# Kernel optimization log

Hardware: AMD Instinct MI355X
Metric: run time of the kernel (lower is better)

The kernel has to match this reference:

```python
import jax, jax.numpy as jnp
import numpy as np

H, D_MODEL, DK, DV = 16, 1024, 64, 64
B, S = 4, 2048
LN_EPS = 1e-6
NEG = -1e9


def setup_inputs() -> dict:
    key = jax.random.key(0)
    ks = jax.random.split(key, 8)
    query = jax.random.normal(ks[0], (B, S, D_MODEL), dtype=jnp.float32)
    k_in = jax.random.normal(ks[1], (B, S, D_MODEL), dtype=jnp.float32)
    v_in = jax.random.normal(ks[2], (B, S, D_MODEL), dtype=jnp.float32)
    mask = jax.random.randint(ks[3], (B, S, S), 0, 2, dtype=jnp.int32)
    sc = 1.0 / np.sqrt(D_MODEL)
    w_qs = jax.random.normal(ks[4], (D_MODEL, H * DK), dtype=jnp.float32) * sc
    w_ks = jax.random.normal(ks[5], (D_MODEL, H * DK), dtype=jnp.float32) * sc
    w_vs = jax.random.normal(ks[6], (D_MODEL, H * DV), dtype=jnp.float32) * sc
    w_out = jax.random.normal(ks[7], (H * DV, D_MODEL), dtype=jnp.float32) * (1.0 / np.sqrt(H * DV))
    ln_g = jnp.ones((D_MODEL,), dtype=jnp.float32)
    ln_b = jnp.zeros((D_MODEL,), dtype=jnp.float32)
    return {"query": query, "key": k_in, "value": v_in, "mask": mask,
            "w_qs": w_qs, "w_ks": w_ks, "w_vs": w_vs, "w_out": w_out,
            "ln_g": ln_g, "ln_b": ln_b}


def reference(query, key, value, mask, w_qs, w_ks, w_vs, w_out, ln_g, ln_b):
    # projections -> [B, H, S, dk/dv]
    q = (query @ w_qs).reshape(B, S, H, DK).transpose(0, 2, 1, 3)
    k = (key @ w_ks).reshape(B, S, H, DK).transpose(0, 2, 1, 3)
    v = (value @ w_vs).reshape(B, S, H, DV).transpose(0, 2, 1, 3)
    scores = jnp.einsum('bhqd,bhkd->bhqk', q, k) / np.sqrt(DK)
    scores = jnp.where(mask[:, None, :, :] == 0, NEG, scores)
    p = jax.nn.softmax(scores, axis=-1)  # dropout = identity in eval
    x = jnp.einsum('bhqk,bhkd->bhqd', p, v)  # [B,H,S,DV]
    x = x.transpose(0, 2, 1, 3).reshape(B, S, H * DV)
    out = x @ w_out + query  # dropout identity, residual
    mu = out.mean(-1, keepdims=True)
    var = out.var(-1, keepdims=True)
    return (out - mu) / jnp.sqrt(var + LN_EPS) * ln_g + ln_b
```

## Files before the change

### kernel.cpp

```cpp
#include <hip/hip_runtime.h>

#define BB   4
#define SS   2048
#define HH   16
#define DM   1024
#define DKV  64
#define LNEPS 1e-6f

#define MD_BF16 0
#define MD_F32  1
#define MD_F16  2

typedef __attribute__((ext_vector_type(8))) short bf16x8;
typedef __attribute__((ext_vector_type(4))) float f32x4;
#define MFMA16(a,b,c) __builtin_amdgcn_mfma_f32_16x16x32_bf16(a,b,c,0,0,0)

__device__ __forceinline__ void gl_lds16(const ushort* g, ushort* l) {
    __builtin_amdgcn_global_load_lds(
        (const __attribute__((address_space(1))) void*)g,
        (__attribute__((address_space(3))) void*)l, 16, 0, 0);
}
__device__ __forceinline__ void wait_vm0_barrier() {
    asm volatile("s_waitcnt vmcnt(0)" ::: "memory");
    __builtin_amdgcn_s_barrier();
}

__device__ __forceinline__ float2 unpack2(unsigned int u) {
    union { unsigned int i; float f; } a, b;
    a.i = u << 16;
    b.i = u & 0xffff0000u;
    return make_float2(a.f, b.f);
}
__device__ __forceinline__ unsigned short f2bf(float f) {
    union { float f; unsigned int i; } c; c.f = f;
    unsigned int u = c.i;
    unsigned int r = u + 0x7fffu + ((u >> 16) & 1u);
    return (unsigned short)(r >> 16);
}
__device__ __forceinline__ unsigned short f2bf_t(float f) {
    union { float f; unsigned int i; } c; c.f = f;
    return (unsigned short)(c.i >> 16);
}
__device__ __forceinline__ float h2f(unsigned int bits16) {
    unsigned short s = (unsigned short)bits16;
    _Float16 x;
    __builtin_memcpy(&x, &s, 2);
    return (float)x;
}
__device__ __forceinline__ void load8m(const void* p, int mode, size_t e0, float* o) {
    if (mode == MD_F32) {
        const float* f = (const float*)p + e0;
        float4 a = *(const float4*)f;
        float4 b = *(const float4*)(f + 4);
        o[0] = a.x; o[1] = a.y; o[2] = a.z; o[3] = a.w;
        o[4] = b.x; o[5] = b.y; o[6] = b.z; o[7] = b.w;
    } else {
        uint4 u = *(const uint4*)((const ushort*)p + e0);
        unsigned v[4] = {u.x, u.y, u.z, u.w};
        if (mode == MD_BF16) {
#pragma unroll
            for (int j = 0; j < 4; ++j) { float2 t = unpack2(v[j]); o[2*j] = t.x; o[2*j+1] = t.y; }
        } else {
#pragma unroll
            for (int j = 0; j < 4; ++j) { o[2*j] = h2f(v[j] & 0xFFFFu); o[2*j+1] = h2f(v[j] >> 16); }
        }
    }
}
__device__ __forceinline__ void load4m(const void* p, int mode, size_t e0, float* o) {
    if (mode == MD_F32) {
        float4 v = *(const float4*)((const float*)p + e0);
        o[0] = v.x; o[1] = v.y; o[2] = v.z; o[3] = v.w;
    } else {
        uint2 u = *(const uint2*)((const ushort*)p + e0);
        if (mode == MD_BF16) {
            float2 a = unpack2(u.x), b = unpack2(u.y);
            o[0] = a.x; o[1] = a.y; o[2] = b.x; o[3] = b.y;
        } else {
            o[0] = h2f(u.x & 0xFFFFu); o[1] = h2f(u.x >> 16);
            o[2] = h2f(u.y & 0xFFFFu); o[3] = h2f(u.y >> 16);
        }
    }
}
__device__ __forceinline__ float loadS(const void* p, int mode, size_t i) {
    if (mode == MD_F32) return ((const float*)p)[i];
    unsigned short u = ((const ushort*)p)[i];
    if (mode == MD_BF16) { union { unsigned i; float f; } c; c.i = (unsigned)u << 16; return c.f; }
    return h2f(u);
}

struct SniffArgs { const void* p[10]; int nhalf[10]; };

__global__ void sniff_all(SniffArgs a, int* __restrict__ modes) {
    __shared__ int cE, cO;
    const int slots[9] = {0, 1, 2, 4, 5, 6, 7, 8, 9};
    const int slot = slots[blockIdx.x];
    const ushort* p = (const ushort*)a.p[slot];
    const int nhalf = a.nhalf[slot];
    if (threadIdx.x == 0) { cE = 0; cO = 0; }
    __syncthreads();
    int e = 0, o = 0;
    for (int i = threadIdx.x; i < nhalf; i += 256) {
        unsigned ex = (p[i] >> 7) & 0xFFu;
        int hit = (ex < 100u || ex == 0xFFu) ? 1 : 0;
        if (i & 1) o += hit; else e += hit;
    }
    atomicAdd(&cE, e);
    atomicAdd(&cO, o);
    __syncthreads();
    if (threadIdx.x == 0) {
        int total = cE + cO;
        modes[slot] = (total < 48) ? MD_BF16 : ((cO * 4 < cE) ? MD_F32 : MD_F16);
    }
}

__global__ __launch_bounds__(256) void mpack(
    const int* __restrict__ mask, unsigned int* __restrict__ pm)
{
    const int w = blockIdx.x * 256 + threadIdx.x;
    const int* p = mask + (size_t)w * 32;
    unsigned int bits = 0u;
#pragma unroll
    for (int j = 0; j < 8; ++j) {
        int4 v = *(const int4*)(p + j * 4);
        bits |= (v.x ? 1u : 0u) << (4 * j);
        bits |= (v.y ? 1u : 0u) << (4 * j + 1);
        bits |= (v.z ? 1u : 0u) << (4 * j + 2);
        bits |= (v.w ? 1u : 0u) << (4 * j + 3);
    }
    pm[w] = bits;
}

__global__ __launch_bounds__(256) void aconv(
    const void* __restrict__ A, ushort* __restrict__ Ab,
    const int* __restrict__ modes, int slot)
{
    const int m = modes[slot];
    const size_t e0 = ((size_t)blockIdx.x * 256 + threadIdx.x) * 16;
    float t[16];
    load8m(A, m, e0, t);
    load8m(A, m, e0 + 8, t + 8);
    union { ushort u[16]; uint4 v[2]; } p;
#pragma unroll
    for (int j = 0; j < 16; ++j) p.u[j] = f2bf(t[j]);
    *(uint4*)&Ab[e0]     = p.v[0];
    *(uint4*)&Ab[e0 + 8] = p.v[1];
}

struct WtArgs { const void* W[3]; ushort* Wt[3]; int slot[3]; };

__device__ __forceinline__ void wtrans_body(
    const void* __restrict__ W, ushort* __restrict__ Wt, int m)
{
    __shared__ ushort T[64][68];
    const int tid = threadIdx.x;
    const int k0 = blockIdx.y * 64, n0 = blockIdx.x * 64;

    const int r = tid >> 2, c = (tid & 3) * 16;
    float t[4];
#pragma unroll
    for (int j = 0; j < 4; ++j) {
        load4m(W, m, (size_t)(k0 + r) * DM + n0 + c + 4 * j, t);
#pragma unroll
        for (int i = 0; i < 4; ++i) T[r][c + 4 * j + i] = f2bf(t[i]);
    }
    __syncthreads();

    const int rn = tid >> 2, ck = (tid & 3) * 16;
    union { ushort u[8]; uint4 v; } p0, p1;
#pragma unroll
    for (int j = 0; j < 8; ++j) { p0.u[j] = T[ck + j][rn]; p1.u[j] = T[ck + 8 + j][rn]; }
    ushort* op = &Wt[(size_t)(n0 + rn) * DM + k0 + ck];
    *(uint4*)op = p0.v;
    *(uint4*)(op + 8) = p1.v;
}

__global__ __launch_bounds__(256) void wtrans3(WtArgs a, const int* __restrict__ modes) {
    const int g = blockIdx.z;
    wtrans_body(a.W[g], a.Wt[g], modes[a.slot[g]]);
}
__global__ __launch_bounds__(256) void wtrans(
    const void* __restrict__ W, ushort* __restrict__ Wt,
    const int* __restrict__ modes, int wslot)
{
    wtrans_body(W, Wt, modes[wslot]);
}

__global__ __launch_bounds__(256) void proj_mfma(
    const ushort* __restrict__ A, const ushort* __restrict__ Wt,
    ushort* __restrict__ Out, int vmode, float scale)
{
    __shared__ __align__(16) ushort Asf[2][4096];
    __shared__ __align__(16) ushort Bsf[2][4096];

    const int tid = threadIdx.x;
    const int lane = tid & 63, wv = tid >> 6;
    const int quad = lane >> 4, L = lane & 15;
    const int bid = blockIdx.y * gridDim.x + blockIdx.x;
    const int swz = (bid & 7) * 64 + (bid >> 3);
    const int m0 = (swz >> 3) * 128, n0 = (swz & 7) * 128;
    const int wm = (wv >> 1) * 64, wn = (wv & 1) * 64;

    const int e0 = (wv * 2 + 0) * 512 + lane * 8;
    const int e1 = (wv * 2 + 1) * 512 + lane * 8;
    const ushort* gA0 = A  + (size_t)(m0 + (e0 >> 5)) * DM + (e0 & 31);
    const ushort* gA1 = A  + (size_t)(m0 + (e1 >> 5)) * DM + (e1 & 31);
    const ushort* gB0 = Wt + (size_t)(n0 + (e0 >> 5)) * DM + (e0 & 31);
    const ushort* gB1 = Wt + (size_t)(n0 + (e1 >> 5)) * DM + (e1 & 31);

    f32x4 acc[4][4];
#pragma unroll
    for (int i = 0; i < 4; ++i)
#pragma unroll
        for (int j = 0; j < 4; ++j) { acc[i][j][0] = 0.f; acc[i][j][1] = 0.f; acc[i][j][2] = 0.f; acc[i][j][3] = 0.f; }

    gl_lds16(gA0, &Asf[0][e0]);
    gl_lds16(gA1, &Asf[0][e1]);
    gl_lds16(gB0, &Bsf[0][e0]);
    gl_lds16(gB1, &Bsf[0][e1]);
    wait_vm0_barrier();

    int cur = 0;
    for (int kt = 0; kt < 31; ++kt) {
        const int kn = (kt + 1) * 32;
        gl_lds16(gA0 + kn, &Asf[cur ^ 1][e0]);
        gl_lds16(gA1 + kn, &Asf[cur ^ 1][e1]);
        gl_lds16(gB0 + kn, &Bsf[cur ^ 1][e0]);
        gl_lds16(gB1 + kn, &Bsf[cur ^ 1][e1]);

        bf16x8 af[4], bfr[4];
#pragma unroll
        for (int tm = 0; tm < 4; ++tm) af[tm] = *(const bf16x8*)&Asf[cur][(wm + tm * 16 + L) * 32 + quad * 8];
#pragma unroll
        for (int tn = 0; tn < 4; ++tn) bfr[tn] = *(const bf16x8*)&Bsf[cur][(wn + tn * 16 + L) * 32 + quad * 8];
#pragma unroll
        for (int tm = 0; tm < 4; ++tm)
#pragma unroll
            for (int tn = 0; tn < 4; ++tn)
                acc[tm][tn] = MFMA16(af[tm], bfr[tn], acc[tm][tn]);

        wait_vm0_barrier();
        cur ^= 1;
    }
    {
        bf16x8 af[4], bfr[4];
#pragma unroll
        for (int tm = 0; tm < 4; ++tm) af[tm] = *(const bf16x8*)&Asf[cur][(wm + tm * 16 + L) * 32 + quad * 8];
#pragma unroll
        for (int tn = 0; tn < 4; ++tn) bfr[tn] = *(const bf16x8*)&Bsf[cur][(wn + tn * 16 + L) * 32 + quad * 8];
#pragma unroll
        for (int tm = 0; tm < 4; ++tm)
#pragma unroll
            for (int tn = 0; tn < 4; ++tn)
                acc[tm][tn] = MFMA16(af[tm], bfr[tn], acc[tm][tn]);
    }

#pragma unroll
    for (int tm = 0; tm < 4; ++tm)
#pragma unroll
        for (int tn = 0; tn < 4; ++tn)
#pragma unroll
            for (int r = 0; r < 4; ++r) {
                const int mm = m0 + wm + tm * 16 + quad * 4 + r;
                const int n = n0 + wn + tn * 16 + L;
                const int b = mm >> 11, s = mm & 2047;
                const int h = n >> 6, d = n & 63;
                const size_t o = vmode
                    ? ((size_t)(b * HH + h) * DKV + d) * SS + s
                    : ((size_t)(b * HH + h) * SS + s) * DKV + d;
                Out[o] = f2bf(acc[tm][tn][r] * scale);
            }
}

__global__ __launch_bounds__(256) void attn_mfma(
    const ushort* __restrict__ Q, const ushort* __restrict__ K,
    const ushort* __restrict__ Vt, const unsigned int* __restrict__ pm,
    ushort* __restrict__ Xo)
{
    __shared__ __align__(16) ushort Ks[64][72];
    __shared__ __align__(16) ushort Vs[64][72];
    __shared__ __align__(16) ushort Ps[64][72];

    const int tid = threadIdx.x;
    const int lane = tid & 63, wv = tid >> 6;
    const int quad = lane >> 4, L = lane & 15;
    const int bid = blockIdx.y * gridDim.x + blockIdx.x;
    const int swz = (bid & 7) * 256 + (bid >> 3);
    const int bh = swz >> 5, b = bh >> 4, h = bh & 15;
    const int q0 = (swz & 31) * 64;

    const ushort* qp = &Q[((size_t)bh * SS + q0 + wv * 16 + L) * DKV + quad * 8];
    const bf16x8 aq0 = *(const bf16x8*)qp;
    const bf16x8 aq1 = *(const bf16x8*)(qp + 32);

    f32x4 O[4];
    float lacc[4];
#pragma unroll
    for (int t = 0; t < 4; ++t) { O[t][0] = 0.f; O[t][1] = 0.f; O[t][2] = 0.f; O[t][3] = 0.f; }
#pragma unroll
    for (int r = 0; r < 4; ++r) lacc[r] = 0.f;

    const int sr = tid >> 2, sg = tid & 3;
    const ushort* kbase = &K[((size_t)bh * SS + sr) * DKV + sg * 16];
    const ushort* vbase = &Vt[((size_t)bh * DKV + sr) * SS + sg * 16];
    const unsigned int* pmr[4];
#pragma unroll
    for (int r = 0; r < 4; ++r)
        pmr[r] = pm + ((size_t)b * SS + q0 + wv * 16 + quad * 4 + r) * 64;

    for (int kt = 0; kt < 32; ++kt) {
        __syncthreads();
        *(uint4*)&Ks[sr][sg * 16]     = *(const uint4*)kbase;
        *(uint4*)&Ks[sr][sg * 16 + 8] = *(const uint4*)(kbase + 8);
        *(uint4*)&Vs[sr][sg * 16]     = *(const uint4*)vbase;
        *(uint4*)&Vs[sr][sg * 16 + 8] = *(const uint4*)(vbase + 8);
        kbase += 64 * DKV;
        vbase += 64;

        uint2 mw[4];
#pragma unroll
        for (int r = 0; r < 4; ++r) mw[r] = *(const uint2*)(pmr[r] + 2 * kt);

        __syncthreads();

        f32x4 sc[4];
        __builtin_amdgcn_s_setprio(1);
#pragma unroll
        for (int t = 0; t < 4; ++t) {
            bf16x8 b0 = *(const bf16x8*)&Ks[t * 16 + L][quad * 8];
            bf16x8 b1 = *(const bf16x8*)&Ks[t * 16 + L][32 + quad * 8];
            f32x4 c; c[0] = 0.f; c[1] = 0.f; c[2] = 0.f; c[3] = 0.f;
            c = MFMA16(aq0, b0, c);
            c = MFMA16(aq1, b1, c);
            sc[t] = c;
        }
        __builtin_amdgcn_s_setprio(0);

#pragma unroll
        for (int r = 0; r < 4; ++r) {
            const unsigned mx = mw[r].x, my = mw[r].y;
#pragma unroll
            for (int t = 0; t < 4; ++t) {
                const float s = fminf(sc[t][r], 30.f);
                const float e = __expf(s);
                const unsigned wsel = (t & 2) ? my : mx;
                const float p = ((wsel >> ((t & 1) * 16 + L)) & 1u) ? e : 0.f;
                lacc[r] += p;
                Ps[wv * 16 + quad * 4 + r][t * 16 + L] = f2bf_t(p);
            }
        }

        bf16x8 ap0 = *(const bf16x8*)&Ps[wv * 16 + L][quad * 8];
        bf16x8 ap1 = *(const bf16x8*)&Ps[wv * 16 + L][32 + quad * 8];
        __builtin_amdgcn_s_setprio(1);
#pragma unroll
        for (int t = 0; t < 4; ++t) {
            bf16x8 v0 = *(const bf16x8*)&Vs[t * 16 + L][quad * 8];
            bf16x8 v1 = *(const bf16x8*)&Vs[t * 16 + L][32 + quad * 8];
            O[t] = MFMA16(ap0, v0, O[t]);
            O[t] = MFMA16(ap1, v1, O[t]);
        }
        __builtin_amdgcn_s_setprio(0);
    }

    float inv[4];
#pragma unroll
    for (int r = 0; r < 4; ++r) {
        float l = lacc[r];
#pragma unroll
        for (int off = 1; off < 16; off <<= 1) l += __shfl_xor(l, off, 64);
        inv[r] = 1.f / l;
    }
#pragma unroll
    for (int t = 0; t < 4; ++t)
#pragma unroll
        for (int r = 0; r < 4; ++r) {
            const int qg = q0 + wv * 16 + quad * 4 + r;
            Xo[((size_t)b * SS + qg) * DM + h * DKV + t * 16 + L] = f2bf(O[t][r] * inv[r]);
        }
}

__global__ __launch_bounds__(256) void oproj_mfma(
    const ushort* __restrict__ Xin, const ushort* __restrict__ Wt,
    const void* __restrict__ Qres, float* __restrict__ Out,
    const int* __restrict__ modes)
{
    __shared__ __align__(16) ushort Asf[2][4096];
    __shared__ __align__(16) ushort Bsf[2][4096];

    const int tid = threadIdx.x;
    const int lane = tid & 63, wv = tid >> 6;
    const int quad = lane >> 4, L = lane & 15;
    const int bid = blockIdx.y * gridDim.x + blockIdx.x;
    const int swz = (bid & 7) * 64 + (bid >> 3);
    const int m0 = (swz >> 3) * 128, n0 = (swz & 7) * 128;
    const int wm = (wv >> 1) * 64, wn = (wv & 1) * 64;
    const int mq = modes[0];

    const int e0 = (wv * 2 + 0) * 512 + lane * 8;
    const int e1 = (wv * 2 + 1) * 512 + lane * 8;
    const ushort* gA0 = Xin + (size_t)(m0 + (e0 >> 5)) * DM + (e0 & 31);
    const ushort* gA1 = Xin + (size_t)(m0 + (e1 >> 5)) * DM + (e1 & 31);
    const ushort* gB0 = Wt  + (size_t)(n0 + (e0 >> 5)) * DM + (e0 & 31);
    const ushort* gB1 = Wt  + (size_t)(n0 + (e1 >> 5)) * DM + (e1 & 31);

    f32x4 acc[4][4];
#pragma unroll
    for (int i = 0; i < 4; ++i)
#pragma unroll
        for (int j = 0; j < 4; ++j) { acc[i][j][0] = 0.f; acc[i][j][1] = 0.f; acc[i][j][2] = 0.f; acc[i][j][3] = 0.f; }

    gl_lds16(gA0, &Asf[0][e0]);
    gl_lds16(gA1, &Asf[0][e1]);
    gl_lds16(gB0, &Bsf[0][e0]);
    gl_lds16(gB1, &Bsf[0][e1]);
    wait_vm0_barrier();

    int cur = 0;
    for (int kt = 0; kt < 31; ++kt) {
        const int kn = (kt + 1) * 32;
        gl_lds16(gA0 + kn, &Asf[cur ^ 1][e0]);
        gl_lds16(gA1 + kn, &Asf[cur ^ 1][e1]);
        gl_lds16(gB0 + kn, &Bsf[cur ^ 1][e0]);
        gl_lds16(gB1 + kn, &Bsf[cur ^ 1][e1]);

        bf16x8 af[4], bfr[4];
#pragma unroll
        for (int tm = 0; tm < 4; ++tm) af[tm] = *(const bf16x8*)&Asf[cur][(wm + tm * 16 + L) * 32 + quad * 8];
#pragma unroll
        for (int tn = 0; tn < 4; ++tn) bfr[tn] = *(const bf16x8*)&Bsf[cur][(wn + tn * 16 + L) * 32 + quad * 8];
#pragma unroll
        for (int tm = 0; tm < 4; ++tm)
#pragma unroll
            for (int tn = 0; tn < 4; ++tn)
                acc[tm][tn] = MFMA16(af[tm], bfr[tn], acc[tm][tn]);

        wait_vm0_barrier();
        cur ^= 1;
    }
    {
        bf16x8 af[4], bfr[4];
#pragma unroll
        for (int tm = 0; tm < 4; ++tm) af[tm] = *(const bf16x8*)&Asf[cur][(wm + tm * 16 + L) * 32 + quad * 8];
#pragma unroll
        for (int tn = 0; tn < 4; ++tn) bfr[tn] = *(const bf16x8*)&Bsf[cur][(wn + tn * 16 + L) * 32 + quad * 8];
#pragma unroll
        for (int tm = 0; tm < 4; ++tm)
#pragma unroll
            for (int tn = 0; tn < 4; ++tn)
                acc[tm][tn] = MFMA16(af[tm], bfr[tn], acc[tm][tn]);
    }

#pragma unroll
    for (int tm = 0; tm < 4; ++tm)
#pragma unroll
        for (int tn = 0; tn < 4; ++tn)
#pragma unroll
            for (int r = 0; r < 4; ++r) {
                const int mm = m0 + wm + tm * 16 + quad * 4 + r;
                const int n = n0 + wn + tn * 16 + L;
                const size_t idx = (size_t)mm * DM + n;
                Out[idx] = acc[tm][tn][r] + loadS(Qres, mq, idx);
            }
}

__global__ __launch_bounds__(256) void ln_k(
    float* __restrict__ Out, const void* __restrict__ G,
    const void* __restrict__ Bt, const int* __restrict__ modes)
{
    const int tid = threadIdx.x, wv = tid >> 6, lane = tid & 63;
    const int row = blockIdx.x * 4 + wv;
    const int mg = modes[8], mb = modes[9];
    const size_t base = (size_t)row * DM + lane * 16;

    float v[16];
    float s = 0.f, q = 0.f;
#pragma unroll
    for (int j = 0; j < 16; j += 4) {
        float4 t = *(const float4*)&Out[base + j];
        v[j] = t.x; v[j+1] = t.y; v[j+2] = t.z; v[j+3] = t.w;
        s += t.x + t.y + t.z + t.w;
        q += t.x*t.x + t.y*t.y + t.z*t.z + t.w*t.w;
    }
#pragma unroll
    for (int off = 1; off < 64; off <<= 1) {
        s += __shfl_xor(s, off, 64);
        q += __shfl_xor(q, off, 64);
    }
    const float mu = s * (1.f / 1024.f);
    const float var = q * (1.f / 1024.f) - mu * mu;
    const float inv = rsqrtf(var + LNEPS);

    float gj[16], bj[16];
#pragma unroll
    for (int j = 0; j < 16; j += 4) {
        load4m(G,  mg, (size_t)lane * 16 + j, gj + j);
        load4m(Bt, mb, (size_t)lane * 16 + j, bj + j);
    }
#pragma unroll
    for (int j = 0; j < 16; j += 4) {
        float4 o;
        o.x = (v[j]   - mu) * inv * gj[j]   + bj[j];
        o.y = (v[j+1] - mu) * inv * gj[j+1] + bj[j+1];
        o.z = (v[j+2] - mu) * inv * gj[j+2] + bj[j+2];
        o.w = (v[j+3] - mu) * inv * gj[j+3] + bj[j+3];
        *(float4*)&Out[base + j] = o;
    }
}

extern "C" void kernel_launch(void* const* d_in, const int* in_sizes, int n_in,
                              void* d_out, int out_size, void* d_ws, size_t ws_size,
                              hipStream_t stream)
{
    const void* query = d_in[0];
    const void* key_i = d_in[1];
    const void* value = d_in[2];
    const int*  mask  = (const int*)d_in[3];
    const void* w_qs  = d_in[4];
    const void* w_ks  = d_in[5];
    const void* w_vs  = d_in[6];
    const void* w_out = d_in[7];
    const void* ln_g  = d_in[8];
    const void* ln_b  = d_in[9];
    float* out = (float*)d_out;

    int* modes = (int*)d_ws;
    const size_t PE = (size_t)BB * HH * SS * DKV;
    ushort* Qw = (ushort*)((char*)d_ws + 256);
    ushort* Kw = Qw + PE;
    ushort* Vw = Kw + PE;
    ushort* Xw = Vw + PE;
    ushort* Abuf = Xw;
    ushort* Wtq  = (ushort*)((char*)d_out + (4  << 20));
    ushort* Wtk  = (ushort*)((char*)d_out + (8  << 20));
    ushort* Wtv  = (ushort*)((char*)d_out + (12 << 20));
    ushort* Wt2  = Qw;
    unsigned int* pmask = (unsigned int*)d_out;

    SniffArgs sa;
    for (int i = 0; i < 10; ++i) {
        sa.p[i] = d_in[i];
        sa.nhalf[i] = in_sizes[i] < 4096 ? in_sizes[i] : 4096;
    }
    sniff_all<<<9, 256, 0, stream>>>(sa, modes);
    mpack<<<2048, 256, 0, stream>>>(mask, pmask);

    WtArgs wa;
    wa.W[0] = w_qs; wa.Wt[0] = Wtq; wa.slot[0] = 4;
    wa.W[1] = w_ks; wa.Wt[1] = Wtk; wa.slot[1] = 5;
    wa.W[2] = w_vs; wa.Wt[2] = Wtv; wa.slot[2] = 6;
    wtrans3<<<dim3(16, 16, 3), 256, 0, stream>>>(wa, modes);

    dim3 gproj(8, 64), gtr(16, 16);

    aconv<<<2048, 256, 0, stream>>>(query, Abuf, modes, 0);
    proj_mfma<<<gproj, 256, 0, stream>>>(Abuf, Wtq, Qw, 0, 0.125f);

    aconv<<<2048, 256, 0, stream>>>(key_i, Abuf, modes, 1);
    proj_mfma<<<gproj, 256, 0, stream>>>(Abuf, Wtk, Kw, 0, 1.0f);

    aconv<<<2048, 256, 0, stream>>>(value, Abuf, modes, 2);
    proj_mfma<<<gproj, 256, 0, stream>>>(Abuf, Wtv, Vw, 1, 1.0f);

    attn_mfma<<<dim3(32, 64), 256, 0, stream>>>(Qw, Kw, Vw, pmask, Xw);

    wtrans<<<gtr, 256, 0, stream>>>(w_out, Wt2, modes, 7);
    oproj_mfma<<<gproj, 256, 0, stream>>>(Xw, Wt2, query, out, modes);
    ln_k<<<2048, 256, 0, stream>>>(out, ln_g, ln_b, modes);
}
```

Measured before the change: 527.1 us.

## Fuse input bf16 conversion into QKV projection and batch three GEMMs in one launch

The separate aconv kernels, which converted each activation tensor to a bf16 buffer, are removed. The projection GEMM now loads raw fp32/bf16/fp16 activations into registers, converts them, and stores them to padded LDS, overlapping the next tile's load with the current MFMAs. The Q, K and V projections run as one launch using grid z, which drops two launches and the bf16 round-trip through global memory. In exchange, the A operand no longer goes through direct global-to-LDS loads, register pressure rises from the 16-float staging, and launch bounds now request 4 blocks per CU.

Result: slower. 541.9 us (+2.8%).

```diff
diff --git a/kernel.cpp b/kernel.cpp
--- a/kernel.cpp
+++ b/kernel.cpp
@@ -46,25 +46,6 @@
     _Float16 x;
     __builtin_memcpy(&x, &s, 2);
     return (float)x;
-}
-__device__ __forceinline__ void load8m(const void* p, int mode, size_t e0, float* o) {
-    if (mode == MD_F32) {
-        const float* f = (const float*)p + e0;
-        float4 a = *(const float4*)f;
-        float4 b = *(const float4*)(f + 4);
-        o[0] = a.x; o[1] = a.y; o[2] = a.z; o[3] = a.w;
-        o[4] = b.x; o[5] = b.y; o[6] = b.z; o[7] = b.w;
-    } else {
-        uint4 u = *(const uint4*)((const ushort*)p + e0);
-        unsigned v[4] = {u.x, u.y, u.z, u.w};
-        if (mode == MD_BF16) {
-#pragma unroll
-            for (int j = 0; j < 4; ++j) { float2 t = unpack2(v[j]); o[2*j] = t.x; o[2*j+1] = t.y; }
-        } else {
-#pragma unroll
-            for (int j = 0; j < 4; ++j) { o[2*j] = h2f(v[j] & 0xFFFFu); o[2*j+1] = h2f(v[j] >> 16); }
-        }
-    }
 }
 __device__ __forceinline__ void load4m(const void* p, int mode, size_t e0, float* o) {
     if (mode == MD_F32) {
@@ -88,6 +69,35 @@
     return h2f(u);
 }
 
+__device__ __forceinline__ void loadAraw(const void* p, int m, size_t e, uint4* r) {
+    if (m == MD_F32) {
+        const float* f = (const float*)p + e;
+        r[0] = *(const uint4*)(f);
+        r[1] = *(const uint4*)(f + 4);
+        r[2] = *(const uint4*)(f + 8);
+        r[3] = *(const uint4*)(f + 12);
+    } else {
+        const ushort* s = (const ushort*)p + e;
+        r[0] = *(const uint4*)s;
+        r[1] = *(const uint4*)(s + 8);
+    }
+}
+__device__ __forceinline__ void cvtA16(const uint4* r, int m, uint4* o2) {
+    union { ushort u[16]; uint4 v[2]; } o;
+    if (m == MD_F32) {
+        const float* f = (const float*)r;
+#pragma unroll
+        for (int j = 0; j < 16; ++j) o.u[j] = f2bf(f[j]);
+    } else if (m == MD_BF16) {
+        o.v[0] = r[0]; o.v[1] = r[1];
+    } else {
+        const ushort* s = (const ushort*)r;
+#pragma unroll
+        for (int j = 0; j < 16; ++j) o.u[j] = f2bf(h2f(s[j]));
+    }
+    o2[0] = o.v[0]; o2[1] = o.v[1];
+}
+
 struct SniffArgs { const void* p[10]; int nhalf[10]; };
 
 __global__ void sniff_all(SniffArgs a, int* __restrict__ modes) {
@@ -130,22 +140,6 @@
     pm[w] = bits;
 }
 
-__global__ __launch_bounds__(256) void aconv(
-    const void* __restrict__ A, ushort* __restrict__ Ab,
-    const int* __restrict__ modes, int slot)
-{
-    const int m = modes[slot];
-    const size_t e0 = ((size_t)blockIdx.x * 256 + threadIdx.x) * 16;
-    float t[16];
-    load8m(A, m, e0, t);
-    load8m(A, m, e0 + 8, t + 8);
-    union { ushort u[16]; uint4 v[2]; } p;
-#pragma unroll
-    for (int j = 0; j < 16; ++j) p.u[j] = f2bf(t[j]);
-    *(uint4*)&Ab[e0]     = p.v[0];
-    *(uint4*)&Ab[e0 + 8] = p.v[1];
-}
-
 struct WtArgs { const void* W[3]; ushort* Wt[3]; int slot[3]; };
 
 __device__ __forceinline__ void wtrans_body(
@@ -185,12 +179,22 @@
     wtrans_body(W, Wt, modes[wslot]);
 }
 
-__global__ __launch_bounds__(256) void proj_mfma(
-    const ushort* __restrict__ A, const ushort* __restrict__ Wt,
-    ushort* __restrict__ Out, int vmode, float scale)
-{
-    __shared__ __align__(16) ushort Asf[2][4096];
-    __shared__ __align__(16) ushort Bsf[2][4096];
+__global__ __launch_bounds__(256, 4) void projqkv(
+    const void* __restrict__ Aq, const void* __restrict__ Ak, const void* __restrict__ Av,
+    const ushort* __restrict__ Wtq, const ushort* __restrict__ Wtk, const ushort* __restrict__ Wtv,
+    ushort* __restrict__ Qo, ushort* __restrict__ Ko, ushort* __restrict__ Vo,
+    const int* __restrict__ modes)
+{
+    __shared__ __align__(16) ushort As[2][128 * 40];
+    __shared__ __align__(16) ushort Bs[2][128 * 32];
+
+    const int z = blockIdx.z;
+    const void* A = (z == 0) ? Aq : (z == 1) ? Ak : Av;
+    const ushort* Wt = (z == 0) ? Wtq : (z == 1) ? Wtk : Wtv;
+    ushort* Out = (z == 0) ? Qo : (z == 1) ? Ko : Vo;
+    const int vmode = (z == 2);
+    const float scale = (z == 0) ? 0.125f : 1.0f;
+    const int m = modes[z];
 
     const int tid = threadIdx.x;
     const int lane = tid & 63, wv = tid >> 6;
@@ -202,51 +206,63 @@
 
     const int e0 = (wv * 2 + 0) * 512 + lane * 8;
     const int e1 = (wv * 2 + 1) * 512 + lane * 8;
-    const ushort* gA0 = A  + (size_t)(m0 + (e0 >> 5)) * DM + (e0 & 31);
-    const ushort* gA1 = A  + (size_t)(m0 + (e1 >> 5)) * DM + (e1 & 31);
     const ushort* gB0 = Wt + (size_t)(n0 + (e0 >> 5)) * DM + (e0 & 31);
     const ushort* gB1 = Wt + (size_t)(n0 + (e1 >> 5)) * DM + (e1 & 31);
 
+    const int arow = tid >> 1, aseg = tid & 1;
+    const size_t aoff = (size_t)(m0 + arow) * DM + aseg * 16;
+    const int alds = arow * 40 + aseg * 16;
+
     f32x4 acc[4][4];
 #pragma unroll
     for (int i = 0; i < 4; ++i)
 #pragma unroll
         for (int j = 0; j < 4; ++j) { acc[i][j][0] = 0.f; acc[i][j][1] = 0.f; acc[i][j][2] = 0.f; acc[i][j][3] = 0.f; }
 
-    gl_lds16(gA0, &Asf[0][e0]);
-    gl_lds16(gA1, &Asf[0][e1]);
-    gl_lds16(gB0, &Bsf[0][e0]);
-    gl_lds16(gB1, &Bsf[0][e1]);
-    wait_vm0_barrier();
+    {
+        gl_lds16(gB0, &Bs[0][e0]);
+        gl_lds16(gB1, &Bs[0][e1]);
+        uint4 ar[4], ao[2];
+        loadAraw(A, m, aoff, ar);
+        cvtA16(ar, m, ao);
+        *(uint4*)&As[0][alds]     = ao[0];
+        *(uint4*)&As[0][alds + 8] = ao[1];
+    }
+    __syncthreads();
 
     int cur = 0;
     for (int kt = 0; kt < 31; ++kt) {
         const int kn = (kt + 1) * 32;
-        gl_lds16(gA0 + kn, &Asf[cur ^ 1][e0]);
-        gl_lds16(gA1 + kn, &Asf[cur ^ 1][e1]);
-        gl_lds16(gB0 + kn, &Bsf[cur ^ 1][e0]);
-        gl_lds16(gB1 + kn, &Bsf[cur ^ 1][e1]);
+        const int nxt = cur ^ 1;
+        gl_lds16(gB0 + kn, &Bs[nxt][e0]);
+        gl_lds16(gB1 + kn, &Bs[nxt][e1]);
+        uint4 ar[4], ao[2];
+        loadAraw(A, m, aoff + kn, ar);
 
         bf16x8 af[4], bfr[4];
 #pragma unroll
-        for (int tm = 0; tm < 4; ++tm) af[tm] = *(const bf16x8*)&Asf[cur][(wm + tm * 16 + L) * 32 + quad * 8];
-#pragma unroll
-        for (int tn = 0; tn < 4; ++tn) bfr[tn] = *(const bf16x8*)&Bsf[cur][(wn + tn * 16 + L) * 32 + quad * 8];
+        for (int tm = 0; tm < 4; ++tm) af[tm] = *(const bf16x8*)&As[cur][(wm + tm * 16 + L) * 40 + quad * 8];
+#pragma unroll
+        for (int tn = 0; tn < 4; ++tn) bfr[tn] = *(const bf16x8*)&Bs[cur][(wn + tn * 16 + L) * 32 + quad * 8];
 #pragma unroll
         for (int tm = 0; tm < 4; ++tm)
 #pragma unroll
             for (int tn = 0; tn < 4; ++tn)
                 acc[tm][tn] = MFMA16(af[tm], bfr[tn], acc[tm][tn]);
 
-        wait_vm0_barrier();
+        cvtA16(ar, m, ao);
+        *(uint4*)&As[nxt][alds]     = ao[0];
+        *(uint4*)&As[nxt][alds + 8] = ao[1];
+
+        __syncthreads();
         cur ^= 1;
     }
     {
         bf16x8 af[4], bfr[4];
 #pragma unroll
-        for (int tm = 0; tm < 4; ++tm) af[tm] = *(const bf16x8*)&Asf[cur][(wm + tm * 16 + L) * 32 + quad * 8];
-#pragma unroll
-        for (int tn = 0; tn < 4; ++tn) bfr[tn] = *(const bf16x8*)&Bsf[cur][(wn + tn * 16 + L) * 32 + quad * 8];
+        for (int tm = 0; tm < 4; ++tm) af[tm] = *(const bf16x8*)&As[cur][(wm + tm * 16 + L) * 40 + quad * 8];
+#pragma unroll
+        for (int tn = 0; tn < 4; ++tn) bfr[tn] = *(const bf16x8*)&Bs[cur][(wn + tn * 16 + L) * 32 + quad * 8];
 #pragma unroll
         for (int tm = 0; tm < 4; ++tm)
 #pragma unroll
@@ -529,7 +545,6 @@
     ushort* Kw = Qw + PE;
     ushort* Vw = Kw + PE;
     ushort* Xw = Vw + PE;
-    ushort* Abuf = Xw;
     ushort* Wtq  = (ushort*)((char*)d_out + (4  << 20));
     ushort* Wtk  = (ushort*)((char*)d_out + (8  << 20));
     ushort* Wtv  = (ushort*)((char*)d_out + (12 << 20));
@@ -550,20 +565,12 @@
     wa.W[2] = w_vs; wa.Wt[2] = Wtv; wa.slot[2] = 6;
     wtrans3<<<dim3(16, 16, 3), 256, 0, stream>>>(wa, modes);
 
-    dim3 gproj(8, 64), gtr(16, 16);
-
-    aconv<<<2048, 256, 0, stream>>>(query, Abuf, modes, 0);
-    proj_mfma<<<gproj, 256, 0, stream>>>(Abuf, Wtq, Qw, 0, 0.125f);
-
-    aconv<<<2048, 256, 0, stream>>>(key_i, Abuf, modes, 1);
-    proj_mfma<<<gproj, 256, 0, stream>>>(Abuf, Wtk, Kw, 0, 1.0f);
-
-    aconv<<<2048, 256, 0, stream>>>(value, Abuf, modes, 2);
-    proj_mfma<<<gproj, 256, 0, stream>>>(Abuf, Wtv, Vw, 1, 1.0f);
+    projqkv<<<dim3(8, 64, 3), 256, 0, stream>>>(
+        query, key_i, value, Wtq, Wtk, Wtv, Qw, Kw, Vw, modes);
 
     attn_mfma<<<dim3(32, 64), 256, 0, stream>>>(Qw, Kw, Vw, pmask, Xw);
 
-    wtrans<<<gtr, 256, 0, stream>>>(w_out, Wt2, modes, 7);
-    oproj_mfma<<<gproj, 256, 0, stream>>>(Xw, Wt2, query, out, modes);
+    wtrans<<<dim3(16, 16), 256, 0, stream>>>(w_out, Wt2, modes, 7);
+    oproj_mfma<<<dim3(8, 64), 256, 0, stream>>>(Xw, Wt2, query, out, modes);
     ln_k<<<2048, 256, 0, stream>>>(out, ln_g, ln_b, modes);
 }
```
